# Optimization experiments

Measured on AMD Instinct MI355X. Metric: run time of the kernel, lower is better.

## Reference

```python
import jax, jax.numpy as jnp
import numpy as np

B, S, D, H = 2, 2048, 1024, 16
HD = D // H  # head_dim = 64
SCALE = 1.0 / np.sqrt(np.float32(D))  # original divides by sqrt(d_keys) == sqrt(d_model)


def setup_inputs() -> dict:
    key = jax.random.key(0)
    ks = jax.random.split(key, 8)
    inp = {
        "query": jax.random.normal(ks[0], (B, S, D), jnp.float32),
        "key": jax.random.normal(ks[1], (B, S, D), jnp.float32),
        "value": jax.random.normal(ks[2], (B, S, D), jnp.float32),
        # nn.Linear weights stored as [out, in]; y = x @ W.T
        "Wq": jax.random.normal(ks[3], (D, D), jnp.float32) * 0.02,
        "Wk": jax.random.normal(ks[4], (D, D), jnp.float32) * 0.02,
        "Wv": jax.random.normal(ks[5], (D, D), jnp.float32) * 0.02,
        "Wo": jax.random.normal(ks[6], (D, D), jnp.float32) * 0.02,
        "bo": jax.random.normal(ks[7], (D,), jnp.float32) * 0.02,
    }
    return inp


def reference(query, key, value, Wq, Wk, Wv, Wo, bo):
    # projections (no bias)
    Q = jnp.einsum('bsd,ed->bse', query, Wq)
    K = jnp.einsum('bsd,ed->bse', key, Wk)
    V = jnp.einsum('bsd,ed->bse', value, Wv)
    # split heads -> [B, H, S, HD]
    Q = Q.reshape(B, S, H, HD).transpose(0, 2, 1, 3)
    K = K.reshape(B, S, H, HD).transpose(0, 2, 1, 3)
    V = V.reshape(B, S, H, HD).transpose(0, 2, 1, 3)
    # scores [B,H,S,S]; note: scaled by 1/sqrt(d_model), matching the source
    scores = jnp.einsum('bhqd,bhkd->bhqk', Q, K) * SCALE
    attn = jax.nn.softmax(scores, axis=-1)  # dropout_ratio=0 -> identity
    ctx = jnp.einsum('bhqk,bhkd->bhqd', attn, V)
    ctx = ctx.transpose(0, 2, 1, 3).reshape(B, S, D)
    return jnp.einsum('bsd,ed->bse', ctx, Wo) + bo
```

## Files before the change

kernel.cpp:

```cpp
#include <hip/hip_runtime.h>
#include <hip/hip_bf16.h>

#define B_  2
#define S_  2048
#define D_  1024
#define H_  16
#define HD_ 64
#define SCALE_ 0.03125f
#define LOG2E_ 1.4426950408889634f
#define QSCALE_ (SCALE_ * LOG2E_)

typedef __bf16 bf16;
typedef __attribute__((ext_vector_type(8))) __bf16 bf16x8;
typedef __attribute__((ext_vector_type(8))) unsigned short u16x8;
typedef __attribute__((ext_vector_type(4))) __bf16 bf16x4;
typedef __attribute__((ext_vector_type(4))) float f32x4;

__device__ __forceinline__ void gload_lds16(const void* g, void* l) {
  __builtin_amdgcn_global_load_lds(
      (const __attribute__((address_space(1))) unsigned int*)g,
      (__attribute__((address_space(3))) unsigned int*)l,
      16, 0, 0);
}

__device__ __forceinline__ bf16x8 load8(const float* p) {
  const float4 a = *(const float4*)p;
  const float4 b = *(const float4*)(p + 4);
  bf16x8 r;
  r[0] = (bf16)a.x; r[1] = (bf16)a.y; r[2] = (bf16)a.z; r[3] = (bf16)a.w;
  r[4] = (bf16)b.x; r[5] = (bf16)b.y; r[6] = (bf16)b.z; r[7] = (bf16)b.w;
  return r;
}
__device__ __forceinline__ bf16x8 load8(const bf16* p) {
  return *(const bf16x8*)p;
}

__global__ __launch_bounds__(256)
void wconv_kernel(const float* __restrict__ Wq, const float* __restrict__ Wk,
                  const float* __restrict__ Wv, const float* __restrict__ Wo,
                  bf16* __restrict__ dst)
{
  const int n4  = (blockIdx.x * 256 + threadIdx.x) * 4;
  const int m   = n4 >> 20;
  const int off = n4 & ((1 << 20) - 1);
  const float* src = m == 0 ? Wq : (m == 1 ? Wk : (m == 2 ? Wv : Wo));
  const float4 a = *(const float4*)(src + off);
  bf16x4 o = {(bf16)a.x, (bf16)a.y, (bf16)a.z, (bf16)a.w};
  *(bf16x4*)(dst + n4) = o;
}

__global__ __launch_bounds__(256)
void conv_kernel(const float* __restrict__ Wq, const float* __restrict__ Wk,
                 const float* __restrict__ Wv, const float* __restrict__ Wo,
                 const float* __restrict__ q, const float* __restrict__ k,
                 const float* __restrict__ v, bf16* __restrict__ dst)
{
  const size_t MI = (size_t)1 << 20;
  const size_t n4 = ((size_t)blockIdx.x * 256 + threadIdx.x) * 4;
  const float* src;
  size_t so, dof;
  if (n4 < 4 * MI) {
    const int m = (int)(n4 >> 20);
    src = m == 0 ? Wq : (m == 1 ? Wk : (m == 2 ? Wv : Wo));
    so  = n4 & (MI - 1);
    dof = n4;
  } else {
    const size_t a = n4 - 4 * MI;
    const int m = (int)(a >> 22);
    src = m == 0 ? q : (m == 1 ? k : v);
    so  = a & (4 * MI - 1);
    dof = n4 + 4 * MI;
  }
  const float4 a4 = *(const float4*)(src + so);
  bf16x4 o = {(bf16)a4.x, (bf16)a4.y, (bf16)a4.z, (bf16)a4.w};
  *(bf16x4*)(dst + dof) = o;
}

__global__ __launch_bounds__(256, 2)
void gemm_qkv3_kernel(const bf16* __restrict__ Ab, const bf16* __restrict__ Wb,
                      bf16* __restrict__ Cq, bf16* __restrict__ Ck,
                      bf16* __restrict__ Cv)
{
  __shared__ bf16 lA[128 * 32];
  __shared__ bf16 lB[128 * 32];

  const int sel = blockIdx.y >> 3;
  const int bn  = blockIdx.y & 7;
  const bf16* A  = Ab + ((size_t)sel << 22);
  const bf16* Bw = Wb + ((size_t)sel << 20);
  bf16*       C  = sel == 0 ? Cq : (sel == 1 ? Ck : Cv);
  const float scale = sel == 0 ? QSCALE_ : 1.0f;

  const int t    = threadIdx.x;
  const int wave = t >> 6;
  const int lane = t & 63;
  const int quad = lane >> 4;
  const int l16  = lane & 15;
  const int bm = blockIdx.x;
  const int wm = (wave >> 1) * 64;
  const int wn = (wave & 1) * 64;

  const int srow = t >> 2;
  const int scol = (t & 3) * 8;
  const bf16* gA = A  + (size_t)(bm * 128 + srow) * D_ + scol;
  const bf16* gB = Bw + (size_t)(bn * 128 + srow) * D_ + scol;

  f32x4 acc[4][4] = {};

  for (int k0 = 0; k0 < D_; k0 += 32) {
    __syncthreads();
    gload_lds16(gA,                   (char*)lA + wave * 1024);
    gload_lds16(gA + (size_t)64 * D_, (char*)lA + 4096 + wave * 1024);
    gload_lds16(gB,                   (char*)lB + wave * 1024);
    gload_lds16(gB + (size_t)64 * D_, (char*)lB + 4096 + wave * 1024);
    __syncthreads();

    bf16x8 af[4], bfr[4];
#pragma unroll
    for (int i = 0; i < 4; ++i) {
      af[i]  = *(const bf16x8*)(lA + (wm + i * 16 + l16) * 32 + quad * 8);
      bfr[i] = *(const bf16x8*)(lB + (wn + i * 16 + l16) * 32 + quad * 8);
    }
#pragma unroll
    for (int mi = 0; mi < 4; ++mi)
#pragma unroll
      for (int ni = 0; ni < 4; ++ni)
        acc[mi][ni] = __builtin_amdgcn_mfma_f32_16x16x32_bf16(
            af[mi], bfr[ni], acc[mi][ni], 0, 0, 0);

    gA += 32;
    gB += 32;
  }

#pragma unroll
  for (int mi = 0; mi < 4; ++mi) {
#pragma unroll
    for (int ni = 0; ni < 4; ++ni) {
      const int col = bn * 128 + wn + ni * 16 + l16;
#pragma unroll
      for (int r = 0; r < 4; ++r) {
        const int row = bm * 128 + wm + mi * 16 + quad * 4 + r;
        C[(size_t)row * D_ + col] = (bf16)(acc[mi][ni][r] * scale);
      }
    }
  }
}

__global__ __launch_bounds__(256, 2)
void gemm_qkv_b_kernel(const float* __restrict__ Aq, const float* __restrict__ Ak,
                       const float* __restrict__ Av, const bf16* __restrict__ Wb,
                       bf16* __restrict__ Cq, bf16* __restrict__ Ck,
                       bf16* __restrict__ Cv)
{
  __shared__ bf16 lA[128 * 32];
  __shared__ bf16 lB[128 * 32];

  const int sel = blockIdx.y >> 3;
  const int bn  = blockIdx.y & 7;
  const float* A  = sel == 0 ? Aq : (sel == 1 ? Ak : Av);
  const bf16*  Bw = Wb + ((size_t)sel << 20);
  bf16*        C  = sel == 0 ? Cq : (sel == 1 ? Ck : Cv);
  const float scale = sel == 0 ? QSCALE_ : 1.0f;

  const int t    = threadIdx.x;
  const int wave = t >> 6;
  const int lane = t & 63;
  const int quad = lane >> 4;
  const int l16  = lane & 15;
  const int bm = blockIdx.x;
  const int wm = (wave >> 1) * 64;
  const int wn = (wave & 1) * 64;

  const int srow = t >> 2;
  const int scol = (t & 3) * 8;
  const float* gA  = A  + (size_t)(bm * 128 + srow) * D_ + scol;
  const bf16*  gBb = Bw + (size_t)(bn * 128 + srow) * D_ + scol;

  f32x4 acc[4][4] = {};

  bf16x8 a0 = load8(gA);
  bf16x8 a1 = load8(gA + (size_t)64 * D_);

  for (int k0 = 0; k0 < D_; k0 += 32) {
    __syncthreads();
    *(bf16x8*)(lA + srow * 32 + scol)        = a0;
    *(bf16x8*)(lA + (srow + 64) * 32 + scol) = a1;
    gload_lds16(gBb,                   (char*)lB + wave * 1024);
    gload_lds16(gBb + (size_t)64 * D_, (char*)lB + 4096 + wave * 1024);
    gBb += 32;
    __syncthreads();

    if (k0 + 32 < D_) {
      gA += 32;
      a0 = load8(gA);
      a1 = load8(gA + (size_t)64 * D_);
    }

    bf16x8 af[4], bfr[4];
#pragma unroll
    for (int i = 0; i < 4; ++i) {
      af[i]  = *(const bf16x8*)(lA + (wm + i * 16 + l16) * 32 + quad * 8);
      bfr[i] = *(const bf16x8*)(lB + (wn + i * 16 + l16) * 32 + quad * 8);
    }
#pragma unroll
    for (int mi = 0; mi < 4; ++mi)
#pragma unroll
      for (int ni = 0; ni < 4; ++ni)
        acc[mi][ni] = __builtin_amdgcn_mfma_f32_16x16x32_bf16(
            af[mi], bfr[ni], acc[mi][ni], 0, 0, 0);
  }

#pragma unroll
  for (int mi = 0; mi < 4; ++mi) {
#pragma unroll
    for (int ni = 0; ni < 4; ++ni) {
      const int col = bn * 128 + wn + ni * 16 + l16;
#pragma unroll
      for (int r = 0; r < 4; ++r) {
        const int row = bm * 128 + wm + mi * 16 + quad * 4 + r;
        C[(size_t)row * D_ + col] = (bf16)(acc[mi][ni][r] * scale);
      }
    }
  }
}

__global__ __launch_bounds__(256, 2)
void gemm_out_b_kernel(const bf16* __restrict__ A, const bf16* __restrict__ Bw,
                       const float* __restrict__ bias, float* __restrict__ C)
{
  __shared__ bf16 lA[128 * 32];
  __shared__ bf16 lB[64 * 32];

  const int t    = threadIdx.x;
  const int wave = t >> 6;
  const int lane = t & 63;
  const int quad = lane >> 4;
  const int l16  = lane & 15;
  const int bm = blockIdx.x;
  const int bn = blockIdx.y;
  const int wm = wave * 32;

  const int srow = t >> 2;
  const int scol = (t & 3) * 8;
  const bf16* gA = A  + (size_t)(bm * 128 + srow) * D_ + scol;
  const bf16* gB = Bw + (size_t)(bn * 64 + srow) * D_ + scol;

  f32x4 acc[2][4] = {};

  for (int k0 = 0; k0 < D_; k0 += 32) {
    __syncthreads();
    gload_lds16(gA,                   (char*)lA + wave * 1024);
    gload_lds16(gA + (size_t)64 * D_, (char*)lA + 4096 + wave * 1024);
    gload_lds16(gB,                   (char*)lB + wave * 1024);
    __syncthreads();

    bf16x8 af[2], bfr[4];
#pragma unroll
    for (int i = 0; i < 2; ++i)
      af[i]  = *(const bf16x8*)(lA + (wm + i * 16 + l16) * 32 + quad * 8);
#pragma unroll
    for (int i = 0; i < 4; ++i)
      bfr[i] = *(const bf16x8*)(lB + (i * 16 + l16) * 32 + quad * 8);
#pragma unroll
    for (int mi = 0; mi < 2; ++mi)
#pragma unroll
      for (int ni = 0; ni < 4; ++ni)
        acc[mi][ni] = __builtin_amdgcn_mfma_f32_16x16x32_bf16(
            af[mi], bfr[ni], acc[mi][ni], 0, 0, 0);

    gA += 32;
    gB += 32;
  }

  float bv[4];
#pragma unroll
  for (int ni = 0; ni < 4; ++ni)
    bv[ni] = bias[bn * 64 + ni * 16 + l16];
#pragma unroll
  for (int mi = 0; mi < 2; ++mi) {
#pragma unroll
    for (int ni = 0; ni < 4; ++ni) {
      const int col = bn * 64 + ni * 16 + l16;
#pragma unroll
      for (int r = 0; r < 4; ++r) {
        const int row = bm * 128 + wm + mi * 16 + quad * 4 + r;
        C[(size_t)row * D_ + col] = acc[mi][ni][r] + bv[ni];
      }
    }
  }
}

__global__ __launch_bounds__(256, 2)
void gemm_qkv_kernel(const float* __restrict__ Aq, const float* __restrict__ Ak,
                     const float* __restrict__ Av, const float* __restrict__ Wq,
                     const float* __restrict__ Wk, const float* __restrict__ Wv,
                     bf16* __restrict__ Cq, bf16* __restrict__ Ck,
                     bf16* __restrict__ Cv)
{
  __shared__ bf16 lA[128 * 32];
  __shared__ bf16 lB[128 * 32];

  const int sel = blockIdx.y >> 3;
  const int bn  = blockIdx.y & 7;
  const float* A  = sel == 0 ? Aq : (sel == 1 ? Ak : Av);
  const float* Bw = sel == 0 ? Wq : (sel == 1 ? Wk : Wv);
  bf16*        C  = sel == 0 ? Cq : (sel == 1 ? Ck : Cv);
  const float scale = sel == 0 ? QSCALE_ : 1.0f;

  const int t    = threadIdx.x;
  const int wave = t >> 6;
  const int lane = t & 63;
  const int quad = lane >> 4;
  const int l16  = lane & 15;
  const int bm = blockIdx.x;
  const int wm = (wave >> 1) * 64;
  const int wn = (wave & 1) * 64;

  const int srow = t >> 2;
  const int scol = (t & 3) * 8;
  const float* gA = A  + (size_t)(bm * 128 + srow) * D_ + scol;
  const float* gB = Bw + (size_t)(bn * 128 + srow) * D_ + scol;

  f32x4 acc[4][4] = {};

  for (int k0 = 0; k0 < D_; k0 += 32) {
    const bf16x8 a0 = load8(gA);
    const bf16x8 a1 = load8(gA + (size_t)64 * D_);
    const bf16x8 b0 = load8(gB);
    const bf16x8 b1 = load8(gB + (size_t)64 * D_);

    __syncthreads();
    *(bf16x8*)(lA + srow * 32 + scol)        = a0;
    *(bf16x8*)(lA + (srow + 64) * 32 + scol) = a1;
    *(bf16x8*)(lB + srow * 32 + scol)        = b0;
    *(bf16x8*)(lB + (srow + 64) * 32 + scol) = b1;
    __syncthreads();

    bf16x8 af[4], bfr[4];
#pragma unroll
    for (int i = 0; i < 4; ++i) {
      af[i]  = *(const bf16x8*)(lA + (wm + i * 16 + l16) * 32 + quad * 8);
      bfr[i] = *(const bf16x8*)(lB + (wn + i * 16 + l16) * 32 + quad * 8);
    }
#pragma unroll
    for (int mi = 0; mi < 4; ++mi)
#pragma unroll
      for (int ni = 0; ni < 4; ++ni)
        acc[mi][ni] = __builtin_amdgcn_mfma_f32_16x16x32_bf16(
            af[mi], bfr[ni], acc[mi][ni], 0, 0, 0);

    gA += 32;
    gB += 32;
  }

#pragma unroll
  for (int mi = 0; mi < 4; ++mi) {
#pragma unroll
    for (int ni = 0; ni < 4; ++ni) {
      const int col = bn * 128 + wn + ni * 16 + l16;
#pragma unroll
      for (int r = 0; r < 4; ++r) {
        const int row = bm * 128 + wm + mi * 16 + quad * 4 + r;
        C[(size_t)row * D_ + col] = (bf16)(acc[mi][ni][r] * scale);
      }
    }
  }
}

__global__ __launch_bounds__(256, 2)
void gemm_out_kernel(const bf16* __restrict__ A, const float* __restrict__ Bw,
                     const float* __restrict__ bias, float* __restrict__ C)
{
  __shared__ bf16 lA[128 * 32];
  __shared__ bf16 lB[64 * 32];

  const int t    = threadIdx.x;
  const int wave = t >> 6;
  const int lane = t & 63;
  const int quad = lane >> 4;
  const int l16  = lane & 15;
  const int bm = blockIdx.x;
  const int bn = blockIdx.y;
  const int wm = wave * 32;

  const int srow = t >> 2;
  const int scol = (t & 3) * 8;
  const bf16*  gA = A  + (size_t)(bm * 128 + srow) * D_ + scol;
  const float* gB = Bw + (size_t)(bn * 64 + srow) * D_ + scol;

  f32x4 acc[2][4] = {};

  for (int k0 = 0; k0 < D_; k0 += 32) {
    const bf16x8 a0 = load8(gA);
    const bf16x8 a1 = load8(gA + (size_t)64 * D_);
    const bf16x8 b0 = load8(gB);

    __syncthreads();
    *(bf16x8*)(lA + srow * 32 + scol)        = a0;
    *(bf16x8*)(lA + (srow + 64) * 32 + scol) = a1;
    *(bf16x8*)(lB + srow * 32 + scol)        = b0;
    __syncthreads();

    bf16x8 af[2], bfr[4];
#pragma unroll
    for (int i = 0; i < 2; ++i)
      af[i]  = *(const bf16x8*)(lA + (wm + i * 16 + l16) * 32 + quad * 8);
#pragma unroll
    for (int i = 0; i < 4; ++i)
      bfr[i] = *(const bf16x8*)(lB + (i * 16 + l16) * 32 + quad * 8);
#pragma unroll
    for (int mi = 0; mi < 2; ++mi)
#pragma unroll
      for (int ni = 0; ni < 4; ++ni)
        acc[mi][ni] = __builtin_amdgcn_mfma_f32_16x16x32_bf16(
            af[mi], bfr[ni], acc[mi][ni], 0, 0, 0);

    gA += 32;
    gB += 32;
  }

  float bv[4];
#pragma unroll
  for (int ni = 0; ni < 4; ++ni)
    bv[ni] = bias[bn * 64 + ni * 16 + l16];
#pragma unroll
  for (int mi = 0; mi < 2; ++mi) {
#pragma unroll
    for (int ni = 0; ni < 4; ++ni) {
      const int col = bn * 64 + ni * 16 + l16;
#pragma unroll
      for (int r = 0; r < 4; ++r) {
        const int row = bm * 128 + wm + mi * 16 + quad * 4 + r;
        C[(size_t)row * D_ + col] = acc[mi][ni][r] + bv[ni];
      }
    }
  }
}

__global__ __launch_bounds__(256, 2)
void attn_kernel(const bf16* Q, const bf16* __restrict__ K,
                 const bf16* __restrict__ V, bf16* O)
{
  __shared__ bf16 lQ[128 * 72];
  __shared__ bf16 lK[2][64 * 72];
  __shared__ bf16 lVT[2][64 * 72];
  __shared__ bf16 lP[4][32 * 72];

  const int t    = threadIdx.x;
  const int wave = t >> 6;
  const int lane = t & 63;
  const int quad = lane >> 4;
  const int l16  = lane & 15;

  const int flat = blockIdx.y * 16 + blockIdx.x;
  const int qt   = (flat >> 3) & 15;
  const int bh   = (flat & 7) * 4 + (flat >> 7);
  const size_t headoff =
      (size_t)(bh >> 4) * ((size_t)S_ * D_) + (size_t)(bh & 15) * HD_;

  const bf16* Kb = K + headoff;
  const bf16* Vb = V + headoff;

  const int sr  = t >> 3;
  const int scx = (t & 7) * 8;
#pragma unroll
  for (int i = 0; i < 4; ++i) {
    const bf16x8 qv =
        *(const bf16x8*)(Q + headoff + (size_t)(qt * 128 + sr + 32 * i) * D_ + scx);
    *(bf16x8*)(lQ + (sr + 32 * i) * 72 + scx) = qv;
  }
  __syncthreads();

  bf16x8 qf[2][2];
#pragma unroll
  for (int m = 0; m < 2; ++m)
#pragma unroll
    for (int ks = 0; ks < 2; ++ks)
      qf[m][ks] = *(const bf16x8*)(lQ + (wave * 32 + m * 16 + l16) * 72 +
                                   (ks * 4 + quad) * 8);

  f32x4 acco[2][4] = {};
  float den[2] = {0.f, 0.f};

  const int dp = t & 31;
  const int kg = t >> 5;

  const int NT = S_ / 64;
  bf16x8 pk0, pk1;
  unsigned int pv[8];

  {
    const bf16* kb = Kb + (size_t)sr * D_ + scx;
    pk0 = load8(kb);
    pk1 = load8(kb + (size_t)32 * D_);
    const bf16* vb = Vb + (size_t)(kg * 8) * D_ + 2 * dp;
#pragma unroll
    for (int j = 0; j < 8; ++j)
      pv[j] = *(const unsigned int*)(vb + (size_t)j * D_);
  }
  {
    *(bf16x8*)(lK[0] + sr * 72 + scx)        = pk0;
    *(bf16x8*)(lK[0] + (sr + 32) * 72 + scx) = pk1;
    u16x8 w0, w1;
#pragma unroll
    for (int j = 0; j < 8; ++j) {
      w0[j] = (unsigned short)(pv[j] & 0xffffu);
      w1[j] = (unsigned short)(pv[j] >> 16);
    }
    *(u16x8*)(lVT[0] + (2 * dp) * 72 + kg * 8)     = w0;
    *(u16x8*)(lVT[0] + (2 * dp + 1) * 72 + kg * 8) = w1;
  }
  {
    const bf16* kb = Kb + (size_t)(64 + sr) * D_ + scx;
    pk0 = load8(kb);
    pk1 = load8(kb + (size_t)32 * D_);
    const bf16* vb = Vb + (size_t)(64 + kg * 8) * D_ + 2 * dp;
#pragma unroll
    for (int j = 0; j < 8; ++j)
      pv[j] = *(const unsigned int*)(vb + (size_t)j * D_);
  }
  __syncthreads();

  for (int kt = 0; kt < NT; ++kt) {
    const int cur = kt & 1;
    bf16* lKc  = lK[cur];
    bf16* lVc  = lVT[cur];

    if (kt + 1 < NT) {
      bf16* lKn = lK[cur ^ 1];
      bf16* lVn = lVT[cur ^ 1];
      *(bf16x8*)(lKn + sr * 72 + scx)        = pk0;
      *(bf16x8*)(lKn + (sr + 32) * 72 + scx) = pk1;
      u16x8 w0, w1;
#pragma unroll
      for (int j = 0; j < 8; ++j) {
        w0[j] = (unsigned short)(pv[j] & 0xffffu);
        w1[j] = (unsigned short)(pv[j] >> 16);
      }
      *(u16x8*)(lVn + (2 * dp) * 72 + kg * 8)     = w0;
      *(u16x8*)(lVn + (2 * dp + 1) * 72 + kg * 8) = w1;
    }

    if (kt + 2 < NT) {
      const bf16* kb = Kb + (size_t)((kt + 2) * 64 + sr) * D_ + scx;
      pk0 = load8(kb);
      pk1 = load8(kb + (size_t)32 * D_);
      const bf16* vb = Vb + (size_t)((kt + 2) * 64 + kg * 8) * D_ + 2 * dp;
#pragma unroll
      for (int j = 0; j < 8; ++j)
        pv[j] = *(const unsigned int*)(vb + (size_t)j * D_);
    }

    f32x4 sc[2][4] = {};
#pragma unroll
    for (int nt = 0; nt < 4; ++nt) {
#pragma unroll
      for (int ks = 0; ks < 2; ++ks) {
        const bf16x8 kf =
            *(const bf16x8*)(lKc + (nt * 16 + l16) * 72 + (ks * 4 + quad) * 8);
#pragma unroll
        for (int m = 0; m < 2; ++m)
          sc[m][nt] = __builtin_amdgcn_mfma_f32_16x16x32_bf16(
              kf, qf[m][ks], sc[m][nt], 0, 0, 0);
      }
    }

    bf16* lPw = lP[wave];
#pragma unroll
    for (int m = 0; m < 2; ++m) {
#pragma unroll
      for (int nt = 0; nt < 4; ++nt) {
        bf16x4 pw;
#pragma unroll
        for (int r = 0; r < 4; ++r) {
          const float p = __builtin_amdgcn_exp2f(sc[m][nt][r]);
          pw[r] = (bf16)p;
          den[m] += p;
        }
        *(bf16x4*)(lPw + (m * 16 + l16) * 72 + nt * 16 + quad * 4) = pw;
      }
    }

    asm volatile("" ::: "memory");
    __builtin_amdgcn_sched_barrier(0);

    bf16x8 pf[2][2];
#pragma unroll
    for (int m = 0; m < 2; ++m)
#pragma unroll
      for (int ks = 0; ks < 2; ++ks)
        pf[m][ks] = *(const bf16x8*)(lPw + (m * 16 + l16) * 72 +
                                     ks * 32 + quad * 8);
#pragma unroll
    for (int dt = 0; dt < 4; ++dt) {
#pragma unroll
      for (int ks = 0; ks < 2; ++ks) {
        const bf16x8 vf =
            *(const bf16x8*)(lVc + (dt * 16 + l16) * 72 + (ks * 4 + quad) * 8);
#pragma unroll
        for (int m = 0; m < 2; ++m)
          acco[m][dt] = __builtin_amdgcn_mfma_f32_16x16x32_bf16(
              pf[m][ks], vf, acco[m][dt], 0, 0, 0);
      }
    }

    __syncthreads();
  }

#pragma unroll
  for (int m = 0; m < 2; ++m) {
    den[m] += __shfl_xor(den[m], 16);
    den[m] += __shfl_xor(den[m], 32);
  }
#pragma unroll
  for (int m = 0; m < 2; ++m) {
#pragma unroll
    for (int r = 0; r < 4; ++r) {
      const float rd  = 1.f / __shfl(den[m], quad * 4 + r);
      const int   row = qt * 128 + wave * 32 + m * 16 + quad * 4 + r;
#pragma unroll
      for (int dt = 0; dt < 4; ++dt)
        O[headoff + (size_t)row * D_ + dt * 16 + l16] =
            (bf16)(acco[m][dt][r] * rd);
    }
  }
}

extern "C" void kernel_launch(void* const* d_in, const int* in_sizes, int n_in,
                              void* d_out, int out_size, void* d_ws, size_t ws_size,
                              hipStream_t stream)
{
  const float* q  = (const float*)d_in[0];
  const float* k  = (const float*)d_in[1];
  const float* v  = (const float*)d_in[2];
  const float* Wq = (const float*)d_in[3];
  const float* Wk = (const float*)d_in[4];
  const float* Wv = (const float*)d_in[5];
  const float* Wo = (const float*)d_in[6];
  const float* bo = (const float*)d_in[7];
  float* outf = (float*)d_out;
  bf16*  outs = (bf16*)d_out;
  bf16*  wsb  = (bf16*)d_ws;

  const size_t MD = (size_t)B_ * S_ * D_;

  dim3 blk(256);
  dim3 gqkv(B_ * S_ / 128, 24);
  dim3 gattn(S_ / 128, B_ * H_);
  dim3 gout(B_ * S_ / 128, D_ / 64);

  bf16* Kp = outs;
  bf16* Vp = outs + MD;

  if (ws_size >= (size_t)40 << 20) {
    bf16* Wb = wsb;
    bf16* Qp = wsb + MD;
    bf16* Ab = wsb + 2 * MD;

    conv_kernel<<<16384, blk, 0, stream>>>(Wq, Wk, Wv, Wo, q, k, v, wsb);
    gemm_qkv3_kernel<<<gqkv, blk, 0, stream>>>(Ab, Wb, Qp, Kp, Vp);
    attn_kernel<<<gattn, blk, 0, stream>>>(Qp, Kp, Vp, Qp);
    gemm_out_b_kernel<<<gout, blk, 0, stream>>>(Qp, Wb + 3 * ((size_t)1 << 20),
                                                bo, outf);
  } else if (ws_size >= (size_t)16 << 20) {
    bf16* Wb = wsb;
    bf16* Qp = wsb + MD;

    wconv_kernel<<<4096, blk, 0, stream>>>(Wq, Wk, Wv, Wo, Wb);
    gemm_qkv_b_kernel<<<gqkv, blk, 0, stream>>>(q, k, v, Wb, Qp, Kp, Vp);
    attn_kernel<<<gattn, blk, 0, stream>>>(Qp, Kp, Vp, Qp);
    gemm_out_b_kernel<<<gout, blk, 0, stream>>>(Qp, Wb + 3 * ((size_t)1 << 20),
                                                bo, outf);
  } else {
    bf16* Qp = wsb;

    gemm_qkv_kernel<<<gqkv, blk, 0, stream>>>(q, k, v, Wq, Wk, Wv,
                                              Qp, Kp, Vp);
    attn_kernel<<<gattn, blk, 0, stream>>>(Qp, Kp, Vp, Qp);
    gemm_out_kernel<<<gout, blk, 0, stream>>>(Qp, Wo, bo, outf);
  }
}
```

Measured before the change: 213.1 us.

## Load K fragments directly from global into registers, drop K LDS staging

The attention kernel no longer stages K tiles through shared memory. Each wave loads its MFMA K fragments straight from global memory into registers, prefetching one tile ahead after the QK^T MFMAs. The P scratch buffer now reuses the Q shared buffer, which cuts LDS use and may raise occupancy. In exchange, every wave fetches the full K tile on its own, so global and L2 traffic for K rises about fourfold, and prefetch latency is only hidden by one iteration of compute.

```diff
diff --git a/kernel.cpp b/kernel.cpp
--- a/kernel.cpp
+++ b/kernel.cpp
@@ -441,10 +441,8 @@
 void attn_kernel(const bf16* Q, const bf16* __restrict__ K,
                  const bf16* __restrict__ V, bf16* O)
 {
-  __shared__ bf16 lQ[128 * 72];
-  __shared__ bf16 lK[2][64 * 72];
+  __shared__ bf16 lQP[128 * 72];
   __shared__ bf16 lVT[2][64 * 72];
-  __shared__ bf16 lP[4][32 * 72];
 
   const int t    = threadIdx.x;
   const int wave = t >> 6;
@@ -467,7 +465,7 @@
   for (int i = 0; i < 4; ++i) {
     const bf16x8 qv =
         *(const bf16x8*)(Q + headoff + (size_t)(qt * 128 + sr + 32 * i) * D_ + scx);
-    *(bf16x8*)(lQ + (sr + 32 * i) * 72 + scx) = qv;
+    *(bf16x8*)(lQP + (sr + 32 * i) * 72 + scx) = qv;
   }
   __syncthreads();
 
@@ -476,7 +474,7 @@
   for (int m = 0; m < 2; ++m)
 #pragma unroll
     for (int ks = 0; ks < 2; ++ks)
-      qf[m][ks] = *(const bf16x8*)(lQ + (wave * 32 + m * 16 + l16) * 72 +
+      qf[m][ks] = *(const bf16x8*)(lQP + (wave * 32 + m * 16 + l16) * 72 +
                                    (ks * 4 + quad) * 8);
 
   f32x4 acco[2][4] = {};
@@ -486,21 +484,20 @@
   const int kg = t >> 5;
 
   const int NT = S_ / 64;
-  bf16x8 pk0, pk1;
+
+  bf16x8 kfr[4][2];
+#pragma unroll
+  for (int nt = 0; nt < 4; ++nt)
+#pragma unroll
+    for (int ks = 0; ks < 2; ++ks)
+      kfr[nt][ks] = load8(Kb + (size_t)(nt * 16 + l16) * D_ + (ks * 4 + quad) * 8);
+
   unsigned int pv[8];
-
   {
-    const bf16* kb = Kb + (size_t)sr * D_ + scx;
-    pk0 = load8(kb);
-    pk1 = load8(kb + (size_t)32 * D_);
     const bf16* vb = Vb + (size_t)(kg * 8) * D_ + 2 * dp;
 #pragma unroll
     for (int j = 0; j < 8; ++j)
       pv[j] = *(const unsigned int*)(vb + (size_t)j * D_);
-  }
-  {
-    *(bf16x8*)(lK[0] + sr * 72 + scx)        = pk0;
-    *(bf16x8*)(lK[0] + (sr + 32) * 72 + scx) = pk1;
     u16x8 w0, w1;
 #pragma unroll
     for (int j = 0; j < 8; ++j) {
@@ -509,28 +506,18 @@
     }
     *(u16x8*)(lVT[0] + (2 * dp) * 72 + kg * 8)     = w0;
     *(u16x8*)(lVT[0] + (2 * dp + 1) * 72 + kg * 8) = w1;
-  }
-  {
-    const bf16* kb = Kb + (size_t)(64 + sr) * D_ + scx;
-    pk0 = load8(kb);
-    pk1 = load8(kb + (size_t)32 * D_);
-    const bf16* vb = Vb + (size_t)(64 + kg * 8) * D_ + 2 * dp;
+    const bf16* vb1 = Vb + (size_t)(64 + kg * 8) * D_ + 2 * dp;
 #pragma unroll
     for (int j = 0; j < 8; ++j)
-      pv[j] = *(const unsigned int*)(vb + (size_t)j * D_);
+      pv[j] = *(const unsigned int*)(vb1 + (size_t)j * D_);
   }
   __syncthreads();
 
   for (int kt = 0; kt < NT; ++kt) {
-    const int cur = kt & 1;
-    bf16* lKc  = lK[cur];
-    bf16* lVc  = lVT[cur];
+    bf16* lVc = lVT[kt & 1];
 
     if (kt + 1 < NT) {
-      bf16* lKn = lK[cur ^ 1];
-      bf16* lVn = lVT[cur ^ 1];
-      *(bf16x8*)(lKn + sr * 72 + scx)        = pk0;
-      *(bf16x8*)(lKn + (sr + 32) * 72 + scx) = pk1;
+      bf16* lVn = lVT[(kt + 1) & 1];
       u16x8 w0, w1;
 #pragma unroll
       for (int j = 0; j < 8; ++j) {
@@ -541,31 +528,33 @@
       *(u16x8*)(lVn + (2 * dp + 1) * 72 + kg * 8) = w1;
     }
 
+    f32x4 sc[2][4] = {};
+#pragma unroll
+    for (int nt = 0; nt < 4; ++nt)
+#pragma unroll
+      for (int ks = 0; ks < 2; ++ks)
+#pragma unroll
+        for (int m = 0; m < 2; ++m)
+          sc[m][nt] = __builtin_amdgcn_mfma_f32_16x16x32_bf16(
+              kfr[nt][ks], qf[m][ks], sc[m][nt], 0, 0, 0);
+
+    if (kt + 1 < NT) {
+      const bf16* kb = Kb + (size_t)((kt + 1) * 64) * D_;
+#pragma unroll
+      for (int nt = 0; nt < 4; ++nt)
+#pragma unroll
+        for (int ks = 0; ks < 2; ++ks)
+          kfr[nt][ks] = load8(kb + (size_t)(nt * 16 + l16) * D_ +
+                              (ks * 4 + quad) * 8);
+    }
     if (kt + 2 < NT) {
-      const bf16* kb = Kb + (size_t)((kt + 2) * 64 + sr) * D_ + scx;
-      pk0 = load8(kb);
-      pk1 = load8(kb + (size_t)32 * D_);
       const bf16* vb = Vb + (size_t)((kt + 2) * 64 + kg * 8) * D_ + 2 * dp;
 #pragma unroll
       for (int j = 0; j < 8; ++j)
         pv[j] = *(const unsigned int*)(vb + (size_t)j * D_);
     }
 
-    f32x4 sc[2][4] = {};
-#pragma unroll
-    for (int nt = 0; nt < 4; ++nt) {
-#pragma unroll
-      for (int ks = 0; ks < 2; ++ks) {
-        const bf16x8 kf =
-            *(const bf16x8*)(lKc + (nt * 16 + l16) * 72 + (ks * 4 + quad) * 8);
-#pragma unroll
-        for (int m = 0; m < 2; ++m)
-          sc[m][nt] = __builtin_amdgcn_mfma_f32_16x16x32_bf16(
-              kf, qf[m][ks], sc[m][nt], 0, 0, 0);
-      }
-    }
-
-    bf16* lPw = lP[wave];
+    bf16* lPw = lQP + wave * (32 * 72);
 #pragma unroll
     for (int m = 0; m < 2; ++m) {
 #pragma unroll
```

After: 229.3 us. 1.08x slower.
